# Kernel optimization log

Hardware: AMD Instinct MI355X
Metric: run time of the kernel (lower is better)

Reference implementation:

```python
import jax, jax.numpy as jnp
import numpy as np
import math

B, S, DIM = 2, 2048, 1024
H, KVH = 16, 4
HD = DIM // H          # 64, head dim
WINDOW = 256           # sliding-window size (0 = global)
ROPE_BASE = 10000.0
EPS = 1e-6


def setup_inputs() -> dict:
    key = jax.random.key(0)
    ks = jax.random.split(key, 6)
    s = 0.02
    return {
        "x": jax.random.normal(ks[0], (B, S, DIM), jnp.float32),
        "Wq": jax.random.normal(ks[1], (DIM, DIM), jnp.float32) * s,
        "Wk": jax.random.normal(ks[2], (KVH * HD, DIM), jnp.float32) * s,
        "Wv": jax.random.normal(ks[3], (KVH * HD, DIM), jnp.float32) * s,
        "Wo": jax.random.normal(ks[4], (DIM, DIM), jnp.float32) * s,
        "q_gain": jnp.ones((H,), jnp.float32),
        "pair_mix": jnp.tile(jnp.eye(2, dtype=jnp.float32), (H // 2, 1, 1))
                    + 0.01 * jax.random.normal(ks[5], (H // 2, 2, 2), jnp.float32),
    }


def _rms_norm(v):
    # F.rms_norm over last dim, no learned weight
    return v * jax.lax.rsqrt(jnp.mean(v * v, axis=-1, keepdims=True) + EPS)


def _rope_tables(seqlen, dtype):
    inv_freq = 1.0 / (ROPE_BASE ** (jnp.arange(0, HD, 2, dtype=jnp.float32) / HD))  # [HD/2]
    t = jnp.arange(seqlen, dtype=jnp.float32)
    freqs = jnp.outer(t, inv_freq)                        # [S, HD/2]
    return jnp.cos(freqs).astype(dtype)[None, None], jnp.sin(freqs).astype(dtype)[None, None]


def _apply_rotary(v, cos, sin):
    half = v.shape[-1] // 2
    v1, v2 = v[..., :half], v[..., half:]
    return jnp.concatenate((v1 * cos + v2 * sin, -v1 * sin + v2 * cos), axis=-1)


def reference(x, Wq, Wk, Wv, Wo, q_gain, pair_mix):
    bsz, seqlen, dim = x.shape
    q = (x @ Wq.T).reshape(bsz, seqlen, H, HD).transpose(0, 2, 1, 3)    # [B,H,S,D]
    k = (x @ Wk.T).reshape(bsz, seqlen, KVH, HD).transpose(0, 2, 1, 3)  # [B,KV,S,D]
    v = (x @ Wv.T).reshape(bsz, seqlen, KVH, HD).transpose(0, 2, 1, 3)

    q = _rms_norm(q)
    k = _rms_norm(k)
    cos, sin = _rope_tables(seqlen, q.dtype)
    q = _apply_rotary(q, cos, sin)
    k = _apply_rotary(k, cos, sin)
    q = q * q_gain.astype(q.dtype)[None, :, None, None]

    # GQA expansion (repeat_interleave over head axis)
    rep = H // KVH
    k_full = jnp.repeat(k, rep, axis=1)  # [B,H,S,D]
    v_full = jnp.repeat(v, rep, axis=1)

    # sliding-window causal mask: attend iff 0 <= i-j < WINDOW
    pos = jnp.arange(seqlen)
    mask = (pos[:, None] >= pos[None, :]) & (pos[:, None] - pos[None, :] < WINDOW)

    scale = 1.0 / math.sqrt(HD)
    scores = jnp.einsum('bhqd,bhkd->bhqk', q, k_full) * scale
    scores = jnp.where(mask[None, None], scores, jnp.finfo(scores.dtype).min)
    att = jax.nn.softmax(scores, axis=-1)
    y = jnp.einsum('bhqk,bhkd->bhqd', att, v_full)  # [B,H,S,D]

    # paired-head mixing: mix each consecutive head pair with a 2x2 matrix
    yp = y.reshape(bsz, H // 2, 2, seqlen, HD)
    y = jnp.einsum('bpitd,poi->bpotd', yp, pair_mix.astype(y.dtype)).reshape(bsz, H, seqlen, HD)

    out = y.transpose(0, 2, 1, 3).reshape(bsz, seqlen, dim) @ Wo.T
    return out
```

## Files before the change

kernel.cpp:

```cpp
#include <hip/hip_runtime.h>
#include <hip/hip_bf16.h>
#include <cstdint>

#define S_LEN 2048
#define QKV_COLS 1536

typedef __bf16 bf16_t;
typedef bf16_t bf16x8 __attribute__((ext_vector_type(8)));
typedef bf16_t bf16x4 __attribute__((ext_vector_type(4)));
typedef float f32x4 __attribute__((ext_vector_type(4)));

typedef __attribute__((address_space(1))) void as1_void;
typedef __attribute__((address_space(3))) void as3_void;

__device__ __forceinline__ void async_load16(const void* g, void* lds) {
  __builtin_amdgcn_global_load_lds(
      (as1_void*)(uintptr_t)g,
      (as3_void*)(uint32_t)(uintptr_t)lds,
      16, 0, 0);
}

__global__ __launch_bounds__(256) void convert_all(
    const float4* __restrict__ x, const float4* __restrict__ wq,
    const float4* __restrict__ wk, const float4* __restrict__ wv,
    const float4* __restrict__ wo, const float* __restrict__ pm,
    bf16x4* __restrict__ xb, bf16x4* __restrict__ wqkvb, bf16x4* __restrict__ wob) {
  int u = blockIdx.x * 256 + threadIdx.x;
  if (u >= 1441792) {
    int off = u - 1441792;
    int flat = off * 4;
    int row = flat >> 10, colf = flat & 1023;
    int col2p = colf & ~64;
    int p = colf >> 7, ii = (colf >> 6) & 1;
    float4 a = wo[(row * 1024 + col2p) >> 2];
    float4 bq = wo[(row * 1024 + (col2p | 64)) >> 2];
    float m0v = pm[p * 4 + ii], m1v = pm[p * 4 + 2 + ii];
    bf16x4 o4;
    o4[0] = (bf16_t)(m0v * a.x + m1v * bq.x);
    o4[1] = (bf16_t)(m0v * a.y + m1v * bq.y);
    o4[2] = (bf16_t)(m0v * a.z + m1v * bq.z);
    o4[3] = (bf16_t)(m0v * a.w + m1v * bq.w);
    wob[off] = o4;
    return;
  }
  const float4* src; bf16x4* dst; int off;
  if (u < 1048576)      { src = x;  dst = xb;             off = u; }
  else if (u < 1310720) { src = wq; dst = wqkvb;          off = u - 1048576; }
  else if (u < 1376256) { src = wk; dst = wqkvb + 262144; off = u - 1310720; }
  else                  { src = wv; dst = wqkvb + 327680; off = u - 1376256; }
  float4 f = src[off];
  bf16x4 o;
  o[0] = (bf16_t)f.x; o[1] = (bf16_t)f.y; o[2] = (bf16_t)f.z; o[3] = (bf16_t)f.w;
  dst[off] = o;
}

__global__ __launch_bounds__(256) void gemm_qkv(
    const bf16_t* __restrict__ A, const bf16_t* __restrict__ B,
    bf16_t* __restrict__ C, bf16_t* __restrict__ vt,
    const float* __restrict__ q_gain, int N, int K) {
  __shared__ bf16_t As[64 * 64];
  __shared__ bf16_t Bs[128 * 64];
  const int tid = threadIdx.x;
  const int lane = tid & 63;
  const int w = tid >> 6;
  const int wm = (w & 1) << 5, wn = (w >> 1) << 6;
  const int m0 = blockIdx.y << 6, n0 = blockIdx.x << 7;
  const int fidx = lane & 15, quad = lane >> 4;
  f32x4 acc[2][4] = {};
  int ra0 = (tid + 0) >> 3,   sa0 = ((tid + 0) & 7) ^ (ra0 & 7);
  int ra1 = (tid + 256) >> 3, sa1 = ((tid + 256) & 7) ^ (ra1 & 7);
  const bf16_t* Ag0 = A + (size_t)(m0 + ra0) * K + sa0 * 8;
  const bf16_t* Ag1 = A + (size_t)(m0 + ra1) * K + sa1 * 8;
  const bf16_t* Bg[4];
#pragma unroll
  for (int j = 0; j < 4; j++) {
    int c = tid + j * 256, r = c >> 3, s = (c & 7) ^ (r & 7);
    Bg[j] = B + (size_t)(n0 + r) * K + s * 8;
  }
  int aoff[2][2], boff[4][2];
#pragma unroll
  for (int mi = 0; mi < 2; mi++) {
    int row = wm + mi * 16 + fidx;
#pragma unroll
    for (int half = 0; half < 2; half++)
      aoff[mi][half] = row * 64 + (((half * 4 + quad) ^ (row & 7)) * 8);
  }
#pragma unroll
  for (int ni = 0; ni < 4; ni++) {
    int row = wn + ni * 16 + fidx;
#pragma unroll
    for (int half = 0; half < 2; half++)
      boff[ni][half] = row * 64 + (((half * 4 + quad) ^ (row & 7)) * 8);
  }
  for (int kt = 0; kt < K; kt += 64) {
    __syncthreads();
    async_load16(Ag0 + kt, As + tid * 8);
    async_load16(Ag1 + kt, As + (tid + 256) * 8);
#pragma unroll
    for (int j = 0; j < 4; j++)
      async_load16(Bg[j] + kt, Bs + (tid + j * 256) * 8);
    __syncthreads();
    bf16x8 af[2][2], bfr[4][2];
#pragma unroll
    for (int mi = 0; mi < 2; mi++)
#pragma unroll
      for (int half = 0; half < 2; half++)
        af[mi][half] = *(const bf16x8*)(As + aoff[mi][half]);
#pragma unroll
    for (int ni = 0; ni < 4; ni++)
#pragma unroll
      for (int half = 0; half < 2; half++)
        bfr[ni][half] = *(const bf16x8*)(Bs + boff[ni][half]);
#pragma unroll
    for (int half = 0; half < 2; half++)
#pragma unroll
      for (int mi = 0; mi < 2; mi++)
#pragma unroll
        for (int ni = 0; ni < 4; ni++)
          acc[mi][ni] = __builtin_amdgcn_mfma_f32_16x16x32_bf16(
              af[mi][half], bfr[ni][half], acc[mi][ni], 0, 0, 0);
  }
  const int hc0 = n0 + wn;
  if (hc0 >= 1280) {
#pragma unroll
    for (int mi = 0; mi < 2; mi++)
#pragma unroll
      for (int ni = 0; ni < 4; ni++) {
        int cg = (hc0 - 1280) + ni * 16 + fidx;
        int g = cg >> 6, dh = cg & 63;
        int srow = m0 + wm + mi * 16 + quad * 4;
        int bb = srow >> 11, si = srow & (S_LEN - 1);
        bf16x4 pack;
#pragma unroll
        for (int r = 0; r < 4; r++) pack[r] = (bf16_t)acc[mi][ni][r];
        *(bf16x4*)(vt + ((size_t)((bb * 4 + g) * 64 + dh)) * S_LEN + si) = pack;
      }
    return;
  }
  float gain = 1.f;
  if (hc0 < 1024) gain = q_gain[hc0 >> 6] * 0.125f;
#pragma unroll
  for (int mi = 0; mi < 2; mi++)
#pragma unroll
    for (int r = 0; r < 4; r++) {
      float ss = 0.f;
#pragma unroll
      for (int ni = 0; ni < 4; ni++) { float t = acc[mi][ni][r]; ss += t * t; }
#pragma unroll
      for (int off = 8; off >= 1; off >>= 1) ss += __shfl_xor(ss, off);
      float scl = rsqrtf(ss * (1.f / 64.f) + 1e-6f);
      int s = (m0 + wm + mi * 16 + quad * 4 + r) & (S_LEN - 1);
#pragma unroll
      for (int ni = 0; ni < 2; ni++) {
        float v1 = acc[mi][ni][r] * scl;
        float v2 = acc[mi][ni + 2][r] * scl;
        float fr = (float)(ni * 16 + fidx);
        float ang = (float)s * __expf(fr * -0.28782313662425575f);
        float sn, cs;
        __sincosf(ang, &sn, &cs);
        acc[mi][ni][r]     = (v1 * cs + v2 * sn) * gain;
        acc[mi][ni + 2][r] = (-v1 * sn + v2 * cs) * gain;
      }
    }
#pragma unroll
  for (int mi = 0; mi < 2; mi++)
#pragma unroll
    for (int ni = 0; ni < 4; ni++)
#pragma unroll
      for (int r = 0; r < 4; r++) {
        int gr = m0 + wm + mi * 16 + quad * 4 + r;
        int gc = n0 + wn + ni * 16 + fidx;
        C[(size_t)gr * N + gc] = (bf16_t)acc[mi][ni][r];
      }
}

__global__ __launch_bounds__(256) void gemm_bt_f32(
    const bf16_t* __restrict__ A, const bf16_t* __restrict__ B,
    float* __restrict__ C, int N, int K) {
  __shared__ bf16_t As[64 * 64];
  __shared__ bf16_t Bs[128 * 64];
  const int tid = threadIdx.x;
  const int lane = tid & 63;
  const int w = tid >> 6;
  const int wm = (w & 1) << 5, wn = (w >> 1) << 6;
  const int m0 = blockIdx.y << 6, n0 = blockIdx.x << 7;
  const int fidx = lane & 15, quad = lane >> 4;
  f32x4 acc[2][4] = {};
  int ra0 = (tid + 0) >> 3,   sa0 = ((tid + 0) & 7) ^ (ra0 & 7);
  int ra1 = (tid + 256) >> 3, sa1 = ((tid + 256) & 7) ^ (ra1 & 7);
  const bf16_t* Ag0 = A + (size_t)(m0 + ra0) * K + sa0 * 8;
  const bf16_t* Ag1 = A + (size_t)(m0 + ra1) * K + sa1 * 8;
  const bf16_t* Bg[4];
#pragma unroll
  for (int j = 0; j < 4; j++) {
    int c = tid + j * 256, r = c >> 3, s = (c & 7) ^ (r & 7);
    Bg[j] = B + (size_t)(n0 + r) * K + s * 8;
  }
  int aoff[2][2], boff[4][2];
#pragma unroll
  for (int mi = 0; mi < 2; mi++) {
    int row = wm + mi * 16 + fidx;
#pragma unroll
    for (int half = 0; half < 2; half++)
      aoff[mi][half] = row * 64 + (((half * 4 + quad) ^ (row & 7)) * 8);
  }
#pragma unroll
  for (int ni = 0; ni < 4; ni++) {
    int row = wn + ni * 16 + fidx;
#pragma unroll
    for (int half = 0; half < 2; half++)
      boff[ni][half] = row * 64 + (((half * 4 + quad) ^ (row & 7)) * 8);
  }
  for (int kt = 0; kt < K; kt += 64) {
    __syncthreads();
    async_load16(Ag0 + kt, As + tid * 8);
    async_load16(Ag1 + kt, As + (tid + 256) * 8);
#pragma unroll
    for (int j = 0; j < 4; j++)
      async_load16(Bg[j] + kt, Bs + (tid + j * 256) * 8);
    __syncthreads();
    bf16x8 af[2][2], bfr[4][2];
#pragma unroll
    for (int mi = 0; mi < 2; mi++)
#pragma unroll
      for (int half = 0; half < 2; half++)
        af[mi][half] = *(const bf16x8*)(As + aoff[mi][half]);
#pragma unroll
    for (int ni = 0; ni < 4; ni++)
#pragma unroll
      for (int half = 0; half < 2; half++)
        bfr[ni][half] = *(const bf16x8*)(Bs + boff[ni][half]);
#pragma unroll
    for (int half = 0; half < 2; half++)
#pragma unroll
      for (int mi = 0; mi < 2; mi++)
#pragma unroll
        for (int ni = 0; ni < 4; ni++)
          acc[mi][ni] = __builtin_amdgcn_mfma_f32_16x16x32_bf16(
              af[mi][half], bfr[ni][half], acc[mi][ni], 0, 0, 0);
  }
#pragma unroll
  for (int mi = 0; mi < 2; mi++)
#pragma unroll
    for (int ni = 0; ni < 4; ni++)
#pragma unroll
      for (int r = 0; r < 4; r++) {
        int gr = m0 + wm + mi * 16 + quad * 4 + r;
        int gc = n0 + wn + ni * 16 + fidx;
        C[(size_t)gr * N + gc] = acc[mi][ni][r];
      }
}

#define FIXMAX 8.0f
#define PST 40
#define OST 72
__global__ __launch_bounds__(256) void attn_mfma(
    const bf16_t* __restrict__ qkv, const bf16_t* __restrict__ vt,
    bf16_t* __restrict__ yb) {
  __shared__ bf16_t plds[4][16 * PST];
  __shared__ bf16_t ob[4][32 * OST];
  const int tid = threadIdx.x, lane = tid & 63, w = tid >> 6;
  const int col = lane & 15, quad = lane >> 4;
  const int q0 = blockIdx.x * 32, g = blockIdx.y, b = blockIdx.z;
  const int h = g * 4 + w;

  bf16x8 qf[2][2];
#pragma unroll
  for (int t = 0; t < 2; t++) {
    const bf16_t* qb =
        qkv + ((size_t)b * S_LEN + q0 + t * 16 + col) * QKV_COLS + h * 64 + quad * 8;
    qf[t][0] = *(const bf16x8*)qb;
    qf[t][1] = *(const bf16x8*)(qb + 32);
  }
  const bf16_t* kbase = qkv + (size_t)b * S_LEN * QKV_COLS + 1024 + g * 64 + quad * 8;
  const bf16_t* vbase = vt + ((size_t)((b * 4 + g) * 64) + col) * S_LEN + quad * 8;

  f32x4 o[2][4] = {};
  float ps[2][4] = {};

  const int c_lo = max(0, (q0 - 255) >> 5);
  const int c_hi = (q0 + 31) >> 5;
  for (int c = c_lo; c <= c_hi; c++) {
    const int k0 = c * 32;
    bf16x8 kf[2][2];
#pragma unroll
    for (int nt = 0; nt < 2; nt++) {
      const bf16_t* kp = kbase + (size_t)(k0 + nt * 16 + col) * QKV_COLS;
      kf[nt][0] = *(const bf16x8*)kp;
      kf[nt][1] = *(const bf16x8*)(kp + 32);
    }
    bf16x8 vf[4];
#pragma unroll
    for (int nt2 = 0; nt2 < 4; nt2++)
      vf[nt2] = *(const bf16x8*)(vbase + (size_t)(nt2 * 16) * S_LEN + k0);

#pragma unroll
    for (int t = 0; t < 2; t++) {
      const int qt0 = q0 + t * 16;
      if (k0 > qt0 + 15) continue;
      f32x4 s[2];
#pragma unroll
      for (int nt = 0; nt < 2; nt++) {
        f32x4 a = {};
        a = __builtin_amdgcn_mfma_f32_16x16x32_bf16(qf[t][0], kf[nt][0], a, 0, 0, 0);
        a = __builtin_amdgcn_mfma_f32_16x16x32_bf16(qf[t][1], kf[nt][1], a, 0, 0, 0);
        s[nt] = a;
      }
      const bool needmask = (k0 + 31 > qt0) || (k0 < qt0 - 224);
      if (needmask) {
#pragma unroll
        for (int r = 0; r < 4; r++) {
          int q = qt0 + quad * 4 + r;
#pragma unroll
          for (int nt = 0; nt < 2; nt++) {
            int k = k0 + nt * 16 + col;
            bool valid = (k <= q) && (q - k < 256);
            float p = valid ? __expf(s[nt][r] - FIXMAX) : 0.f;
            ps[t][r] += p;
            plds[w][(quad * 4 + r) * PST + nt * 16 + col] = (bf16_t)p;
          }
        }
      } else {
#pragma unroll
        for (int r = 0; r < 4; r++) {
#pragma unroll
          for (int nt = 0; nt < 2; nt++) {
            float p = __expf(s[nt][r] - FIXMAX);
            ps[t][r] += p;
            plds[w][(quad * 4 + r) * PST + nt * 16 + col] = (bf16_t)p;
          }
        }
      }
      asm volatile("s_waitcnt lgkmcnt(0)" ::: "memory");
      bf16x8 pf = *(const bf16x8*)(plds[w] + col * PST + quad * 8);
#pragma unroll
      for (int nt2 = 0; nt2 < 4; nt2++)
        o[t][nt2] = __builtin_amdgcn_mfma_f32_16x16x32_bf16(pf, vf[nt2], o[t][nt2], 0, 0, 0);
    }
  }
#pragma unroll
  for (int t = 0; t < 2; t++)
#pragma unroll
    for (int r = 0; r < 4; r++) {
      float v = ps[t][r];
#pragma unroll
      for (int off = 8; off >= 1; off >>= 1) v += __shfl_xor(v, off);
      float il = 1.f / v;
      int row = t * 16 + quad * 4 + r;
#pragma unroll
      for (int nt2 = 0; nt2 < 4; nt2++)
        ob[w][row * OST + nt2 * 16 + col] = (bf16_t)(o[t][nt2][r] * il);
    }
  asm volatile("s_waitcnt lgkmcnt(0)" ::: "memory");
#pragma unroll
  for (int it = 0; it < 4; it++) {
    int row = it * 8 + (lane >> 3);
    int d0 = (lane & 7) * 8;
    bf16x8 v8 = *(const bf16x8*)(ob[w] + row * OST + d0);
    *(bf16x8*)(yb + ((size_t)b * S_LEN + q0 + row) * 1024 + h * 64 + d0) = v8;
  }
}

extern "C" void kernel_launch(void* const* d_in, const int* in_sizes, int n_in,
                              void* d_out, int out_size, void* d_ws, size_t ws_size,
                              hipStream_t stream) {
  const float* x        = (const float*)d_in[0];
  const float* Wq       = (const float*)d_in[1];
  const float* Wk       = (const float*)d_in[2];
  const float* Wv       = (const float*)d_in[3];
  const float* Wo       = (const float*)d_in[4];
  const float* q_gain   = (const float*)d_in[5];
  const float* pair_mix = (const float*)d_in[6];
  float* out = (float*)d_out;

  bf16_t* ws    = (bf16_t*)d_ws;
  bf16_t* xb    = ws;
  bf16_t* wqkvb = xb + 4096 * 1024;
  bf16_t* wob   = wqkvb + 1536 * 1024;
  bf16_t* qkvb  = wob + 1024 * 1024;
  bf16_t* yb    = qkvb + 4096 * 1536;
  bf16_t* vt    = yb + 4096 * 1024;

  convert_all<<<6656, 256, 0, stream>>>(
      (const float4*)x, (const float4*)Wq, (const float4*)Wk, (const float4*)Wv,
      (const float4*)Wo, pair_mix, (bf16x4*)xb, (bf16x4*)wqkvb, (bf16x4*)wob);
  gemm_qkv<<<dim3(12, 64), 256, 0, stream>>>(xb, wqkvb, qkvb, vt, q_gain, 1536, 1024);
  attn_mfma<<<dim3(64, 4, 2), 256, 0, stream>>>(qkvb, vt, yb);
  gemm_bt_f32<<<dim3(8, 64), 256, 0, stream>>>(yb, wob, out, 1024, 1024);
}
```

Before: 143.2 us.

## Enlarge GEMM tiles to 128x128 and remap block IDs for XCD locality

Both GEMMs move from 64x128 to 128x128 block tiles, giving each wave a 64x64 output sub-tile with 4x4 MFMA accumulators. This raises arithmetic intensity per LDS load and halves the grid. All three main kernels also remap linear block IDs so that consecutive blocks on the same XCD (orig&7) cover neighbouring tiles, aiming at better L2 reuse. The trade-offs are higher register pressure, fewer blocks (384 and 256) for the 256 CUs, and possible wave-quantization imbalance.

```diff
diff --git a/kernel.cpp b/kernel.cpp
--- a/kernel.cpp
+++ b/kernel.cpp
@@ -58,63 +58,56 @@
     const bf16_t* __restrict__ A, const bf16_t* __restrict__ B,
     bf16_t* __restrict__ C, bf16_t* __restrict__ vt,
     const float* __restrict__ q_gain, int N, int K) {
-  __shared__ bf16_t As[64 * 64];
+  __shared__ bf16_t As[128 * 64];
   __shared__ bf16_t Bs[128 * 64];
   const int tid = threadIdx.x;
   const int lane = tid & 63;
   const int w = tid >> 6;
-  const int wm = (w & 1) << 5, wn = (w >> 1) << 6;
-  const int m0 = blockIdx.y << 6, n0 = blockIdx.x << 7;
+  const int wm = (w & 1) << 6, wn = (w >> 1) << 6;
+  const int orig = blockIdx.y * gridDim.x + blockIdx.x;
+  const int id = (orig & 7) * 48 + (orig >> 3);
+  const int m0 = (id / 12) << 7, n0 = (id % 12) << 7;
   const int fidx = lane & 15, quad = lane >> 4;
-  f32x4 acc[2][4] = {};
-  int ra0 = (tid + 0) >> 3,   sa0 = ((tid + 0) & 7) ^ (ra0 & 7);
-  int ra1 = (tid + 256) >> 3, sa1 = ((tid + 256) & 7) ^ (ra1 & 7);
-  const bf16_t* Ag0 = A + (size_t)(m0 + ra0) * K + sa0 * 8;
-  const bf16_t* Ag1 = A + (size_t)(m0 + ra1) * K + sa1 * 8;
+  f32x4 acc[4][4] = {};
+  const bf16_t* Ag[4];
   const bf16_t* Bg[4];
 #pragma unroll
   for (int j = 0; j < 4; j++) {
     int c = tid + j * 256, r = c >> 3, s = (c & 7) ^ (r & 7);
+    Ag[j] = A + (size_t)(m0 + r) * K + s * 8;
     Bg[j] = B + (size_t)(n0 + r) * K + s * 8;
   }
-  int aoff[2][2], boff[4][2];
-#pragma unroll
-  for (int mi = 0; mi < 2; mi++) {
-    int row = wm + mi * 16 + fidx;
-#pragma unroll
-    for (int half = 0; half < 2; half++)
-      aoff[mi][half] = row * 64 + (((half * 4 + quad) ^ (row & 7)) * 8);
-  }
-#pragma unroll
-  for (int ni = 0; ni < 4; ni++) {
-    int row = wn + ni * 16 + fidx;
-#pragma unroll
-    for (int half = 0; half < 2; half++)
-      boff[ni][half] = row * 64 + (((half * 4 + quad) ^ (row & 7)) * 8);
+  int aoff[4][2], boff[4][2];
+#pragma unroll
+  for (int i = 0; i < 4; i++) {
+    int arow = wm + i * 16 + fidx;
+    int brow = wn + i * 16 + fidx;
+#pragma unroll
+    for (int half = 0; half < 2; half++) {
+      aoff[i][half] = arow * 64 + (((half * 4 + quad) ^ (arow & 7)) * 8);
+      boff[i][half] = brow * 64 + (((half * 4 + quad) ^ (brow & 7)) * 8);
+    }
   }
   for (int kt = 0; kt < K; kt += 64) {
     __syncthreads();
-    async_load16(Ag0 + kt, As + tid * 8);
-    async_load16(Ag1 + kt, As + (tid + 256) * 8);
-#pragma unroll
-    for (int j = 0; j < 4; j++)
+#pragma unroll
+    for (int j = 0; j < 4; j++) {
+      async_load16(Ag[j] + kt, As + (tid + j * 256) * 8);
       async_load16(Bg[j] + kt, Bs + (tid + j * 256) * 8);
+    }
     __syncthreads();
-    bf16x8 af[2][2], bfr[4][2];
-#pragma unroll
-    for (int mi = 0; mi < 2; mi++)
-#pragma unroll
-      for (int half = 0; half < 2; half++)
-        af[mi][half] = *(const bf16x8*)(As + aoff[mi][half]);
-#pragma unroll
-    for (int ni = 0; ni < 4; ni++)
-#pragma unroll
-      for (int half = 0; half < 2; half++)
-        bfr[ni][half] = *(const bf16x8*)(Bs + boff[ni][half]);
+    bf16x8 af[4][2], bfr[4][2];
+#pragma unroll
+    for (int i = 0; i < 4; i++)
+#pragma unroll
+      for (int half = 0; half < 2; half++) {
+        af[i][half]  = *(const bf16x8*)(As + aoff[i][half]);
+        bfr[i][half] = *(const bf16x8*)(Bs + boff[i][half]);
+      }
 #pragma unroll
     for (int half = 0; half < 2; half++)
 #pragma unroll
-      for (int mi = 0; mi < 2; mi++)
+      for (int mi = 0; mi < 4; mi++)
 #pragma unroll
         for (int ni = 0; ni < 4; ni++)
           acc[mi][ni] = __builtin_amdgcn_mfma_f32_16x16x32_bf16(
@@ -123,7 +116,7 @@
   const int hc0 = n0 + wn;
   if (hc0 >= 1280) {
 #pragma unroll
-    for (int mi = 0; mi < 2; mi++)
+    for (int mi = 0; mi < 4; mi++)
 #pragma unroll
       for (int ni = 0; ni < 4; ni++) {
         int cg = (hc0 - 1280) + ni * 16 + fidx;
@@ -140,7 +133,7 @@
   float gain = 1.f;
   if (hc0 < 1024) gain = q_gain[hc0 >> 6] * 0.125f;
 #pragma unroll
-  for (int mi = 0; mi < 2; mi++)
+  for (int mi = 0; mi < 4; mi++)
 #pragma unroll
     for (int r = 0; r < 4; r++) {
       float ss = 0.f;
@@ -163,7 +156,7 @@
       }
     }
 #pragma unroll
-  for (int mi = 0; mi < 2; mi++)
+  for (int mi = 0; mi < 4; mi++)
 #pragma unroll
     for (int ni = 0; ni < 4; ni++)
 #pragma unroll
@@ -177,70 +170,63 @@
 __global__ __launch_bounds__(256) void gemm_bt_f32(
     const bf16_t* __restrict__ A, const bf16_t* __restrict__ B,
     float* __restrict__ C, int N, int K) {
-  __shared__ bf16_t As[64 * 64];
+  __shared__ bf16_t As[128 * 64];
   __shared__ bf16_t Bs[128 * 64];
   const int tid = threadIdx.x;
   const int lane = tid & 63;
   const int w = tid >> 6;
-  const int wm = (w & 1) << 5, wn = (w >> 1) << 6;
-  const int m0 = blockIdx.y << 6, n0 = blockIdx.x << 7;
+  const int wm = (w & 1) << 6, wn = (w >> 1) << 6;
+  const int orig = blockIdx.y * gridDim.x + blockIdx.x;
+  const int id = (orig & 7) * 32 + (orig >> 3);
+  const int m0 = (id >> 3) << 7, n0 = (id & 7) << 7;
   const int fidx = lane & 15, quad = lane >> 4;
-  f32x4 acc[2][4] = {};
-  int ra0 = (tid + 0) >> 3,   sa0 = ((tid + 0) & 7) ^ (ra0 & 7);
-  int ra1 = (tid + 256) >> 3, sa1 = ((tid + 256) & 7) ^ (ra1 & 7);
-  const bf16_t* Ag0 = A + (size_t)(m0 + ra0) * K + sa0 * 8;
-  const bf16_t* Ag1 = A + (size_t)(m0 + ra1) * K + sa1 * 8;
+  f32x4 acc[4][4] = {};
+  const bf16_t* Ag[4];
   const bf16_t* Bg[4];
 #pragma unroll
   for (int j = 0; j < 4; j++) {
     int c = tid + j * 256, r = c >> 3, s = (c & 7) ^ (r & 7);
+    Ag[j] = A + (size_t)(m0 + r) * K + s * 8;
     Bg[j] = B + (size_t)(n0 + r) * K + s * 8;
   }
-  int aoff[2][2], boff[4][2];
-#pragma unroll
-  for (int mi = 0; mi < 2; mi++) {
-    int row = wm + mi * 16 + fidx;
-#pragma unroll
-    for (int half = 0; half < 2; half++)
-      aoff[mi][half] = row * 64 + (((half * 4 + quad) ^ (row & 7)) * 8);
-  }
-#pragma unroll
-  for (int ni = 0; ni < 4; ni++) {
-    int row = wn + ni * 16 + fidx;
-#pragma unroll
-    for (int half = 0; half < 2; half++)
-      boff[ni][half] = row * 64 + (((half * 4 + quad) ^ (row & 7)) * 8);
+  int aoff[4][2], boff[4][2];
+#pragma unroll
+  for (int i = 0; i < 4; i++) {
+    int arow = wm + i * 16 + fidx;
+    int brow = wn + i * 16 + fidx;
+#pragma unroll
+    for (int half = 0; half < 2; half++) {
+      aoff[i][half] = arow * 64 + (((half * 4 + quad) ^ (arow & 7)) * 8);
+      boff[i][half] = brow * 64 + (((half * 4 + quad) ^ (brow & 7)) * 8);
+    }
   }
   for (int kt = 0; kt < K; kt += 64) {
     __syncthreads();
-    async_load16(Ag0 + kt, As + tid * 8);
-    async_load16(Ag1 + kt, As + (tid + 256) * 8);
-#pragma unroll
-    for (int j = 0; j < 4; j++)
+#pragma unroll
+    for (int j = 0; j < 4; j++) {
+      async_load16(Ag[j] + kt, As + (tid + j * 256) * 8);
       async_load16(Bg[j] + kt, Bs + (tid + j * 256) * 8);
+    }
     __syncthreads();
-    bf16x8 af[2][2], bfr[4][2];
-#pragma unroll
-    for (int mi = 0; mi < 2; mi++)
-#pragma unroll
-      for (int half = 0; half < 2; half++)
-        af[mi][half] = *(const bf16x8*)(As + aoff[mi][half]);
-#pragma unroll
-    for (int ni = 0; ni < 4; ni++)
-#pragma unroll
-      for (int half = 0; half < 2; half++)
-        bfr[ni][half] = *(const bf16x8*)(Bs + boff[ni][half]);
+    bf16x8 af[4][2], bfr[4][2];
+#pragma unroll
+    for (int i = 0; i < 4; i++)
+#pragma unroll
+      for (int half = 0; half < 2; half++) {
+        af[i][half]  = *(const bf16x8*)(As + aoff[i][half]);
+        bfr[i][half] = *(const bf16x8*)(Bs + boff[i][half]);
+      }
 #pragma unroll
     for (int half = 0; half < 2; half++)
 #pragma unroll
-      for (int mi = 0; mi < 2; mi++)
+      for (int mi = 0; mi < 4; mi++)
 #pragma unroll
         for (int ni = 0; ni < 4; ni++)
           acc[mi][ni] = __builtin_amdgcn_mfma_f32_16x16x32_bf16(
               af[mi][half], bfr[ni][half], acc[mi][ni], 0, 0, 0);
   }
 #pragma unroll
-  for (int mi = 0; mi < 2; mi++)
+  for (int mi = 0; mi < 4; mi++)
 #pragma unroll
     for (int ni = 0; ni < 4; ni++)
 #pragma unroll
@@ -261,7 +247,9 @@
   __shared__ bf16_t ob[4][32 * OST];
   const int tid = threadIdx.x, lane = tid & 63, w = tid >> 6;
   const int col = lane & 15, quad = lane >> 4;
-  const int q0 = blockIdx.x * 32, g = blockIdx.y, b = blockIdx.z;
+  const int orig = blockIdx.z * 256 + blockIdx.y * 64 + blockIdx.x;
+  const int id = (orig & 7) * 64 + (orig >> 3);
+  const int q0 = (id & 63) * 32, g = (id >> 6) & 3, b = id >> 8;
   const int h = g * 4 + w;
 
   bf16x8 qf[2][2];
@@ -384,7 +372,7 @@
   convert_all<<<6656, 256, 0, stream>>>(
       (const float4*)x, (const float4*)Wq, (const float4*)Wk, (const float4*)Wv,
       (const float4*)Wo, pair_mix, (bf16x4*)xb, (bf16x4*)wqkvb, (bf16x4*)wob);
-  gemm_qkv<<<dim3(12, 64), 256, 0, stream>>>(xb, wqkvb, qkvb, vt, q_gain, 1536, 1024);
+  gemm_qkv<<<dim3(12, 32), 256, 0, stream>>>(xb, wqkvb, qkvb, vt, q_gain, 1536, 1024);
   attn_mfma<<<dim3(64, 4, 2), 256, 0, stream>>>(qkvb, vt, yb);
-  gemm_bt_f32<<<dim3(8, 64), 256, 0, stream>>>(yb, wob, out, 1024, 1024);
-}
+  gemm_bt_f32<<<dim3(8, 32), 256, 0, stream>>>(yb, wob, out, 1024, 1024);
+}
```

After: 153.0 us. +6.8%, slower.
